# Kernel tuning notes

Hardware: AMD Instinct MI355X
Metric: run time of the kernel (lower is better)

## Reference

```python
import jax, jax.numpy as jnp
import numpy as np

D_MODEL = 1024
NUM_HEADS = 16
HEAD_DIM = D_MODEL // NUM_HEADS  # 64


def setup_inputs() -> dict:
    key = jax.random.key(0)
    ks = jax.random.split(key, 9)
    s = 1.0 / np.sqrt(D_MODEL)
    return {
        "x": jax.random.normal(ks[0], (2, 2048, D_MODEL), dtype=jnp.float32),
        "Wq": jax.random.normal(ks[1], (D_MODEL, D_MODEL), dtype=jnp.float32) * s,
        "bq": jnp.zeros((D_MODEL,), dtype=jnp.float32),
        "Wk": jax.random.normal(ks[2], (D_MODEL, HEAD_DIM), dtype=jnp.float32) * s,
        "bk": jnp.zeros((HEAD_DIM,), dtype=jnp.float32),
        "Wv": jax.random.normal(ks[3], (D_MODEL, HEAD_DIM), dtype=jnp.float32) * s,
        "bv": jnp.zeros((HEAD_DIM,), dtype=jnp.float32),
        "Wo": jax.random.normal(ks[4], (D_MODEL, D_MODEL), dtype=jnp.float32) * s,
        "bo": jnp.zeros((D_MODEL,), dtype=jnp.float32),
    }


def reference(x, Wq, bq, Wk, bk, Wv, bv, Wo, bo):
    B, S, D = x.shape
    H, hd = NUM_HEADS, HEAD_DIM
    # Projections: Q has H heads, K/V a single shared head (MQA).
    Q = (x @ Wq + bq).reshape(B, S, H, hd).transpose(0, 2, 1, 3)  # [B,H,S,hd]
    K = x @ Wk + bk  # [B,S,hd]
    V = x @ Wv + bv  # [B,S,hd]
    # Shared-K/V attention: broadcast K across heads instead of expand().
    scores = jnp.einsum("bhqd,bkd->bhqk", Q, K) / np.sqrt(hd)  # [B,H,S,S]
    attn = jax.nn.softmax(scores, axis=-1)
    attended = jnp.einsum("bhqk,bkd->bhqd", attn, V)  # [B,H,S,hd]
    attended = attended.transpose(0, 2, 1, 3).reshape(B, S, D)
    return attended @ Wo + bo
```

## Files before the change

### kernel.cpp

```cpp
#include <hip/hip_runtime.h>
#include <hip/hip_bf16.h>

#define D_MODEL 1024
#define NHEADS  16
#define HD      64
#define BATCH   2
#define SEQ     2048
#define MROWS   4096
#define NQKV    1152
#define NSPLIT  2

typedef short  short4v __attribute__((ext_vector_type(4)));
typedef short  short8  __attribute__((ext_vector_type(8)));
typedef float  floatx4 __attribute__((ext_vector_type(4)));

__device__ inline short f2bf(float f) {
  unsigned u = __builtin_bit_cast(unsigned, f);
  u = (u + 0x7FFF + ((u >> 16) & 1)) >> 16;
  return (short)u;
}

__device__ inline unsigned pack_trunc(float lo, float hi) {
  return __builtin_amdgcn_perm(__builtin_bit_cast(unsigned, hi),
                               __builtin_bit_cast(unsigned, lo), 0x07060302u);
}

__device__ inline void async_copy16(const short* g, short* l) {
  __builtin_amdgcn_global_load_lds(
      (const __attribute__((address_space(1))) unsigned int*)g,
      (__attribute__((address_space(3))) unsigned int*)l, 16, 0, 0);
}

__global__ __launch_bounds__(256)
void prep_kernel(const float* __restrict__ x,  const float* __restrict__ Wq,
                 const float* __restrict__ Wk, const float* __restrict__ Wv,
                 const float* __restrict__ Wo, const float* __restrict__ bq,
                 const float* __restrict__ bk, const float* __restrict__ bv,
                 short* __restrict__ xb, short* __restrict__ Wqkv_t,
                 short* __restrict__ Wo_t, float* __restrict__ bqkv) {
  const int id = blockIdx.x;
  const int t  = threadIdx.x;
  if (id < 544) {
    __shared__ short Ts[64 * 72];
    const float* src; short* dst; int N, off, tile;
    if (id < 256)      { src = Wq; dst = Wqkv_t; N = 1024; off = 0;    tile = id; }
    else if (id < 272) { src = Wk; dst = Wqkv_t; N = 64;   off = 1024; tile = id - 256; }
    else if (id < 288) { src = Wv; dst = Wqkv_t; N = 64;   off = 1088; tile = id - 272; }
    else               { src = Wo; dst = Wo_t;   N = 1024; off = 0;    tile = id - 288; }
    const int k0 = (N == 1024) ? (tile & 15) * 64 : tile * 64;
    const int n0 = (N == 1024) ? (tile >> 4) * 64 : 0;
    {
      const int r = t >> 2, c = (t & 3) * 16;
      const float* s = src + (size_t)(k0 + r) * N + n0 + c;
#pragma unroll
      for (int j = 0; j < 16; j += 4) {
        float4 v = *reinterpret_cast<const float4*>(s + j);
        Ts[r * 72 + c + j + 0] = f2bf(v.x); Ts[r * 72 + c + j + 1] = f2bf(v.y);
        Ts[r * 72 + c + j + 2] = f2bf(v.z); Ts[r * 72 + c + j + 3] = f2bf(v.w);
      }
    }
    __syncthreads();
    {
      const int n = t >> 2, kc = (t & 3) * 16;
      short8 o0, o1;
#pragma unroll
      for (int j = 0; j < 8; ++j) o0[j] = Ts[(kc + j) * 72 + n];
#pragma unroll
      for (int j = 0; j < 8; ++j) o1[j] = Ts[(kc + 8 + j) * 72 + n];
      short* d = dst + (size_t)(off + n0 + n) * 1024 + k0 + kc;
      *reinterpret_cast<short8*>(d)     = o0;
      *reinterpret_cast<short8*>(d + 8) = o1;
    }
  } else if (id < 549) {
    const int i = (id - 544) * 256 + t;
    if (i < 1024)      bqkv[i] = bq[i];
    else if (i < 1088) bqkv[i] = bk[i - 1024];
    else if (i < 1152) bqkv[i] = bv[i - 1088];
  } else {
    const int i = ((id - 549) * 256 + t) * 8;
    if (i < MROWS * D_MODEL) {
      float4 a = *reinterpret_cast<const float4*>(x + i);
      float4 b = *reinterpret_cast<const float4*>(x + i + 4);
      short8 o;
      o[0] = f2bf(a.x); o[1] = f2bf(a.y); o[2] = f2bf(a.z); o[3] = f2bf(a.w);
      o[4] = f2bf(b.x); o[5] = f2bf(b.y); o[6] = f2bf(b.z); o[7] = f2bf(b.w);
      *reinterpret_cast<short8*>(xb + i) = o;
    }
  }
}

template<bool OUT_BF16, int SCALE_N, bool VT_FUSE>
__global__ __launch_bounds__(256)
void gemm_mfma_bt(const short* __restrict__ A, const short* __restrict__ Bt,
                  const float* __restrict__ bias, void* __restrict__ Cout,
                  short* __restrict__ Vtg, int M, int N, int K) {
  __shared__ short As[128 * 64];
  __shared__ short Bs[64 * 64];
  const int t    = threadIdx.x;
  const int w    = t >> 6;
  const int lane = t & 63;
  const int quad = lane >> 4;
  const int l16  = lane & 15;
  const int bm   = blockIdx.x * 128;
  const int bn   = blockIdx.y * 64;
  const int wm   = (w >> 1) * 64;
  const int wn   = (w & 1) * 32;

  const int srow = t >> 3;
  const int cc   = ((t & 7) ^ (srow & 7)) * 8;
  const short* gA = A  + (size_t)(bm + srow) * K + cc;
  const short* gB = Bt + (size_t)(bn + srow) * K + cc;
  short* lA = As + t * 8;
  short* lB = Bs + t * 8;

  floatx4 acc[4][2];
#pragma unroll
  for (int i = 0; i < 4; ++i)
#pragma unroll
    for (int j = 0; j < 2; ++j) acc[i][j] = (floatx4){0.f, 0.f, 0.f, 0.f};

  const int xr = l16 & 7;

  for (int k0 = 0; k0 < K; k0 += 64) {
    __syncthreads();
    async_copy16(gA + k0, lA);
    async_copy16(gA + (size_t)32 * K + k0, lA + 2048);
    async_copy16(gA + (size_t)64 * K + k0, lA + 4096);
    async_copy16(gA + (size_t)96 * K + k0, lA + 6144);
    async_copy16(gB + k0, lB);
    async_copy16(gB + (size_t)32 * K + k0, lB + 2048);
    __syncthreads();

    short8 fa0[4], fa1[4], fb0[2], fb1[2];
#pragma unroll
    for (int mi = 0; mi < 4; ++mi) {
      const int row = wm + mi * 16 + l16;
      fa0[mi] = *reinterpret_cast<const short8*>(&As[row * 64 + (quad ^ xr) * 8]);
      fa1[mi] = *reinterpret_cast<const short8*>(&As[row * 64 + ((4 + quad) ^ xr) * 8]);
    }
#pragma unroll
    for (int ni = 0; ni < 2; ++ni) {
      const int row = wn + ni * 16 + l16;
      fb0[ni] = *reinterpret_cast<const short8*>(&Bs[row * 64 + (quad ^ xr) * 8]);
      fb1[ni] = *reinterpret_cast<const short8*>(&Bs[row * 64 + ((4 + quad) ^ xr) * 8]);
    }
#pragma unroll
    for (int mi = 0; mi < 4; ++mi)
#pragma unroll
      for (int ni = 0; ni < 2; ++ni) {
        acc[mi][ni] = __builtin_amdgcn_mfma_f32_16x16x32_bf16(fa0[mi], fb0[ni], acc[mi][ni], 0, 0, 0);
        acc[mi][ni] = __builtin_amdgcn_mfma_f32_16x16x32_bf16(fa1[mi], fb1[ni], acc[mi][ni], 0, 0, 0);
      }
  }

#pragma unroll
  for (int ni = 0; ni < 2; ++ni) {
    const int col = bn + wn + ni * 16 + l16;
    const float bs = bias[col];
    const float sc = (col < SCALE_N) ? 0.18033688f : 1.0f;
#pragma unroll
    for (int mi = 0; mi < 4; ++mi) {
      const int row = bm + wm + mi * 16 + quad * 4;
      short4v vt4;
#pragma unroll
      for (int r = 0; r < 4; ++r) {
        const float v = (acc[mi][ni][r] + bs) * sc;
        if (OUT_BF16) {
          const short bv16 = f2bf(v);
          ((short*)Cout)[(size_t)(row + r) * N + col] = bv16;
          if (VT_FUSE) vt4[r] = bv16;
        } else {
          ((float*)Cout)[(size_t)(row + r) * N + col] = v;
        }
      }
      if (VT_FUSE && col >= 1088) {
        const int d = col - 1088;
        const int b = row >> 11, s = row & 2047;
        *reinterpret_cast<short4v*>(&Vtg[(size_t)(b * 64 + d) * SEQ + s]) = vt4;
      }
    }
  }
}

__global__ __launch_bounds__(256, 2)
void mqa_flash_bf16(const short* __restrict__ QKV, const short* __restrict__ Vtg,
                    _Float16* __restrict__ Opart, float* __restrict__ lpart) {
  const int bh    = blockIdx.y;
  const int b     = bh >> 4;
  const int h     = bh & 15;
  const int s0    = blockIdx.x * 256;
  const int split = blockIdx.z;
  const int t     = threadIdx.x;
  const int w     = t >> 6;
  const int lane  = t & 63;
  const int quad  = lane >> 4;
  const int l16   = lane & 15;

  __shared__ short KVs[8192];
  __shared__ short Ps[4 * 16 * 72];
  short* Ks   = KVs;
  short* Vt   = KVs + 4096;
  short* myPs = Ps + w * 16 * 72;

  short8 aq[4][2];
#pragma unroll
  for (int st = 0; st < 4; ++st) {
    const short* qrow = &QKV[(size_t)(b * SEQ + s0 + w * 64 + st * 16 + l16) * NQKV + h * HD];
    aq[st][0] = *reinterpret_cast<const short8*>(qrow + quad * 8);
    aq[st][1] = *reinterpret_cast<const short8*>(qrow + 32 + quad * 8);
  }

  floatx4 oacc[4][4];
  floatx4 lacc[4];
#pragma unroll
  for (int st = 0; st < 4; ++st) {
    lacc[st] = (floatx4){0.f, 0.f, 0.f, 0.f};
#pragma unroll
    for (int dg = 0; dg < 4; ++dg) oacc[st][dg] = (floatx4){0.f, 0.f, 0.f, 0.f};
  }

  short8 ones;
#pragma unroll
  for (int j = 0; j < 8; ++j) ones[j] = (short)0x3F80;

  const int srow = t >> 3;
  const int cc   = ((t & 7) ^ (srow & 7)) * 8;
  const short* gK0 = QKV + (size_t)(b * SEQ + srow) * NQKV + 1024 + cc;
  const short* gK1 = gK0 + (size_t)32 * NQKV;
  const short* gV0 = Vtg + (size_t)(b * 64 + srow) * SEQ + cc;
  const short* gV1 = gV0 + (size_t)32 * SEQ;
  short* lK0 = Ks + w * 512;
  short* lK1 = Ks + 2048 + w * 512;
  short* lV0 = Vt + w * 512;
  short* lV1 = Vt + 2048 + w * 512;

  const int xr = l16 & 7;
  const int kbase = split * (SEQ / NSPLIT);

  for (int kk = kbase; kk < kbase + SEQ / NSPLIT; kk += 64) {
    __syncthreads();
    async_copy16(gK0 + (size_t)kk * NQKV, lK0);
    async_copy16(gK1 + (size_t)kk * NQKV, lK1);
    async_copy16(gV0 + kk, lV0);
    async_copy16(gV1 + kk, lV1);
    __syncthreads();

    short8 kb[4][2], vb[4][2];
#pragma unroll
    for (int kg = 0; kg < 4; ++kg) {
      kb[kg][0] = *reinterpret_cast<const short8*>(&Ks[(kg * 16 + l16) * 64 + (quad ^ xr) * 8]);
      kb[kg][1] = *reinterpret_cast<const short8*>(&Ks[(kg * 16 + l16) * 64 + ((4 + quad) ^ xr) * 8]);
    }
#pragma unroll
    for (int dg = 0; dg < 4; ++dg) {
      vb[dg][0] = *reinterpret_cast<const short8*>(&Vt[(dg * 16 + l16) * 64 + (quad ^ xr) * 8]);
      vb[dg][1] = *reinterpret_cast<const short8*>(&Vt[(dg * 16 + l16) * 64 + ((4 + quad) ^ xr) * 8]);
    }

#pragma unroll
    for (int st = 0; st < 4; ++st) {
#pragma unroll
      for (int kg = 0; kg < 4; ++kg) {
        floatx4 s4 = (floatx4){0.f, 0.f, 0.f, 0.f};
        s4 = __builtin_amdgcn_mfma_f32_16x16x32_bf16(kb[kg][0], aq[st][0], s4, 0, 0, 0);
        s4 = __builtin_amdgcn_mfma_f32_16x16x32_bf16(kb[kg][1], aq[st][1], s4, 0, 0, 0);
        float p0 = __builtin_exp2f(s4[0]);
        float p1 = __builtin_exp2f(s4[1]);
        float p2 = __builtin_exp2f(s4[2]);
        float p3 = __builtin_exp2f(s4[3]);
        uint2 pk;
        pk.x = pack_trunc(p0, p1);
        pk.y = pack_trunc(p2, p3);
        *reinterpret_cast<uint2*>(&myPs[l16 * 72 + kg * 16 + quad * 4]) = pk;
      }
      short8 ap0 = *reinterpret_cast<const short8*>(&myPs[l16 * 72 + quad * 8]);
      short8 ap1 = *reinterpret_cast<const short8*>(&myPs[l16 * 72 + 32 + quad * 8]);
      lacc[st] = __builtin_amdgcn_mfma_f32_16x16x32_bf16(ap0, ones, lacc[st], 0, 0, 0);
      lacc[st] = __builtin_amdgcn_mfma_f32_16x16x32_bf16(ap1, ones, lacc[st], 0, 0, 0);
#pragma unroll
      for (int dg = 0; dg < 4; ++dg) {
        oacc[st][dg] = __builtin_amdgcn_mfma_f32_16x16x32_bf16(ap0, vb[dg][0], oacc[st][dg], 0, 0, 0);
        oacc[st][dg] = __builtin_amdgcn_mfma_f32_16x16x32_bf16(ap1, vb[dg][1], oacc[st][dg], 0, 0, 0);
      }
    }
  }

#pragma unroll
  for (int st = 0; st < 4; ++st) {
#pragma unroll
    for (int rg = 0; rg < 4; ++rg) {
      const int qg = s0 + w * 64 + st * 16 + quad * 4 + rg;
      _Float16* dst = Opart + ((size_t)(split * 32 + bh) * SEQ + qg) * 64 + l16;
#pragma unroll
      for (int dg = 0; dg < 4; ++dg) dst[dg * 16] = (_Float16)oacc[st][dg][rg];
      if (l16 == 0) lpart[(size_t)(split * 32 + bh) * SEQ + qg] = lacc[st][rg];
    }
  }
}

__global__ __launch_bounds__(256)
void combine_kernel(const _Float16* __restrict__ Opart, const float* __restrict__ lpart,
                    short* __restrict__ Att) {
  const int idx = blockIdx.x * 256 + threadIdx.x;
  const int r   = idx >> 3;
  const int d0  = (idx & 7) * 8;
  float l = 0.f;
  float o[8] = {0.f,0.f,0.f,0.f,0.f,0.f,0.f,0.f};
#pragma unroll
  for (int s = 0; s < NSPLIT; ++s) {
    const _Float16* op = Opart + ((size_t)(s * 32 * SEQ) + r) * 64 + d0;
    l += lpart[(size_t)s * 32 * SEQ + r];
#pragma unroll
    for (int j = 0; j < 8; ++j) o[j] += (float)op[j];
  }
  const float inv = 1.0f / l;
  short8 ov;
#pragma unroll
  for (int j = 0; j < 8; ++j) ov[j] = f2bf(o[j] * inv);
  const int bhh = r >> 11, q = r & 2047;
  const int bb = bhh >> 4, hh = bhh & 15;
  *reinterpret_cast<short8*>(&Att[(size_t)(bb * SEQ + q) * D_MODEL + hh * HD + d0]) = ov;
}

extern "C" void kernel_launch(void* const* d_in, const int* in_sizes, int n_in,
                              void* d_out, int out_size, void* d_ws, size_t ws_size,
                              hipStream_t stream) {
  const float* x  = (const float*)d_in[0];
  const float* Wq = (const float*)d_in[1];
  const float* bq = (const float*)d_in[2];
  const float* Wk = (const float*)d_in[3];
  const float* bk = (const float*)d_in[4];
  const float* Wv = (const float*)d_in[5];
  const float* bv = (const float*)d_in[6];
  const float* Wo = (const float*)d_in[7];
  const float* bo = (const float*)d_in[8];
  float* out = (float*)d_out;

  short* Wqkv_t = (short*)d_ws;
  short* Wo_t   = Wqkv_t + (size_t)NQKV * D_MODEL;
  short* xb     = Wo_t + (size_t)D_MODEL * D_MODEL;
  short* QKV    = xb + (size_t)MROWS * D_MODEL;
  short* Att    = QKV + (size_t)MROWS * NQKV;
  short* Vtg    = Att + (size_t)MROWS * D_MODEL;
  float* bqkv   = (float*)(Vtg + (size_t)BATCH * HD * SEQ);
  float* lpart  = bqkv + 1152;
  _Float16* Opart = (_Float16*)(lpart + (size_t)NSPLIT * 32 * SEQ);

  prep_kernel<<<2597, 256, 0, stream>>>(x, Wq, Wk, Wv, Wo, bq, bk, bv,
                                        xb, Wqkv_t, Wo_t, bqkv);

  gemm_mfma_bt<true, 1024, true><<<dim3(MROWS / 128, NQKV / 64), 256, 0, stream>>>(
      xb, Wqkv_t, bqkv, QKV, Vtg, MROWS, NQKV, D_MODEL);

  mqa_flash_bf16<<<dim3(SEQ / 256, BATCH * NHEADS, NSPLIT), 256, 0, stream>>>(
      QKV, Vtg, Opart, lpart);

  combine_kernel<<<2048, 256, 0, stream>>>(Opart, lpart, Att);

  gemm_mfma_bt<false, 0, false><<<dim3(MROWS / 128, D_MODEL / 64), 256, 0, stream>>>(
      Att, Wo_t, bo, out, nullptr, MROWS, D_MODEL, D_MODEL);
}
```

Before: 182.9 us.

## Replace split-K attention and combine kernel with smaller query tiles

Drops the two-way split over the key dimension and its separate combine kernel. Each attention block now covers 128 queries instead of 256 and walks the full key sequence, normalizing and writing bf16 output directly. Launch bounds rise to 4 blocks per CU so the reduced per-thread accumulator state allows more occupancy. This removes the fp16 partial writes, the extra launch and the combine pass, but each K/V tile loaded into LDS is now reused by fewer query rows.

```diff
diff --git a/kernel.cpp b/kernel.cpp
--- a/kernel.cpp
+++ b/kernel.cpp
@@ -8,7 +8,6 @@
 #define SEQ     2048
 #define MROWS   4096
 #define NQKV    1152
-#define NSPLIT  2
 
 typedef short  short4v __attribute__((ext_vector_type(4)));
 typedef short  short8  __attribute__((ext_vector_type(8)));
@@ -182,14 +181,13 @@
   }
 }
 
-__global__ __launch_bounds__(256, 2)
+__global__ __launch_bounds__(256, 4)
 void mqa_flash_bf16(const short* __restrict__ QKV, const short* __restrict__ Vtg,
-                    _Float16* __restrict__ Opart, float* __restrict__ lpart) {
+                    short* __restrict__ Att) {
   const int bh    = blockIdx.y;
   const int b     = bh >> 4;
   const int h     = bh & 15;
-  const int s0    = blockIdx.x * 256;
-  const int split = blockIdx.z;
+  const int s0    = blockIdx.x * 128;
   const int t     = threadIdx.x;
   const int w     = t >> 6;
   const int lane  = t & 63;
@@ -202,18 +200,18 @@
   short* Vt   = KVs + 4096;
   short* myPs = Ps + w * 16 * 72;
 
-  short8 aq[4][2];
-#pragma unroll
-  for (int st = 0; st < 4; ++st) {
-    const short* qrow = &QKV[(size_t)(b * SEQ + s0 + w * 64 + st * 16 + l16) * NQKV + h * HD];
+  short8 aq[2][2];
+#pragma unroll
+  for (int st = 0; st < 2; ++st) {
+    const short* qrow = &QKV[(size_t)(b * SEQ + s0 + w * 32 + st * 16 + l16) * NQKV + h * HD];
     aq[st][0] = *reinterpret_cast<const short8*>(qrow + quad * 8);
     aq[st][1] = *reinterpret_cast<const short8*>(qrow + 32 + quad * 8);
   }
 
-  floatx4 oacc[4][4];
-  floatx4 lacc[4];
-#pragma unroll
-  for (int st = 0; st < 4; ++st) {
+  floatx4 oacc[2][4];
+  floatx4 lacc[2];
+#pragma unroll
+  for (int st = 0; st < 2; ++st) {
     lacc[st] = (floatx4){0.f, 0.f, 0.f, 0.f};
 #pragma unroll
     for (int dg = 0; dg < 4; ++dg) oacc[st][dg] = (floatx4){0.f, 0.f, 0.f, 0.f};
@@ -235,9 +233,8 @@
   short* lV1 = Vt + 2048 + w * 512;
 
   const int xr = l16 & 7;
-  const int kbase = split * (SEQ / NSPLIT);
-
-  for (int kk = kbase; kk < kbase + SEQ / NSPLIT; kk += 64) {
+
+  for (int kk = 0; kk < SEQ; kk += 64) {
     __syncthreads();
     async_copy16(gK0 + (size_t)kk * NQKV, lK0);
     async_copy16(gK1 + (size_t)kk * NQKV, lK1);
@@ -258,7 +255,7 @@
     }
 
 #pragma unroll
-    for (int st = 0; st < 4; ++st) {
+    for (int st = 0; st < 2; ++st) {
 #pragma unroll
       for (int kg = 0; kg < 4; ++kg) {
         floatx4 s4 = (floatx4){0.f, 0.f, 0.f, 0.f};
@@ -286,40 +283,17 @@
   }
 
 #pragma unroll
-  for (int st = 0; st < 4; ++st) {
+  for (int st = 0; st < 2; ++st) {
 #pragma unroll
     for (int rg = 0; rg < 4; ++rg) {
-      const int qg = s0 + w * 64 + st * 16 + quad * 4 + rg;
-      _Float16* dst = Opart + ((size_t)(split * 32 + bh) * SEQ + qg) * 64 + l16;
-#pragma unroll
-      for (int dg = 0; dg < 4; ++dg) dst[dg * 16] = (_Float16)oacc[st][dg][rg];
-      if (l16 == 0) lpart[(size_t)(split * 32 + bh) * SEQ + qg] = lacc[st][rg];
-    }
-  }
-}
-
-__global__ __launch_bounds__(256)
-void combine_kernel(const _Float16* __restrict__ Opart, const float* __restrict__ lpart,
-                    short* __restrict__ Att) {
-  const int idx = blockIdx.x * 256 + threadIdx.x;
-  const int r   = idx >> 3;
-  const int d0  = (idx & 7) * 8;
-  float l = 0.f;
-  float o[8] = {0.f,0.f,0.f,0.f,0.f,0.f,0.f,0.f};
-#pragma unroll
-  for (int s = 0; s < NSPLIT; ++s) {
-    const _Float16* op = Opart + ((size_t)(s * 32 * SEQ) + r) * 64 + d0;
-    l += lpart[(size_t)s * 32 * SEQ + r];
-#pragma unroll
-    for (int j = 0; j < 8; ++j) o[j] += (float)op[j];
-  }
-  const float inv = 1.0f / l;
-  short8 ov;
-#pragma unroll
-  for (int j = 0; j < 8; ++j) ov[j] = f2bf(o[j] * inv);
-  const int bhh = r >> 11, q = r & 2047;
-  const int bb = bhh >> 4, hh = bhh & 15;
-  *reinterpret_cast<short8*>(&Att[(size_t)(bb * SEQ + q) * D_MODEL + hh * HD + d0]) = ov;
+      const float inv = 1.0f / lacc[st][rg];
+      const int qg = s0 + w * 32 + st * 16 + quad * 4 + rg;
+      short* dst = &Att[(size_t)(b * SEQ + qg) * D_MODEL + h * HD + l16];
+#pragma unroll
+      for (int dg = 0; dg < 4; ++dg)
+        dst[dg * 16] = f2bf(oacc[st][dg][rg] * inv);
+    }
+  }
 }
 
 extern "C" void kernel_launch(void* const* d_in, const int* in_sizes, int n_in,
@@ -343,8 +317,6 @@
   short* Att    = QKV + (size_t)MROWS * NQKV;
   short* Vtg    = Att + (size_t)MROWS * D_MODEL;
   float* bqkv   = (float*)(Vtg + (size_t)BATCH * HD * SEQ);
-  float* lpart  = bqkv + 1152;
-  _Float16* Opart = (_Float16*)(lpart + (size_t)NSPLIT * 32 * SEQ);
 
   prep_kernel<<<2597, 256, 0, stream>>>(x, Wq, Wk, Wv, Wo, bq, bk, bv,
                                         xb, Wqkv_t, Wo_t, bqkv);
@@ -352,10 +324,7 @@
   gemm_mfma_bt<true, 1024, true><<<dim3(MROWS / 128, NQKV / 64), 256, 0, stream>>>(
       xb, Wqkv_t, bqkv, QKV, Vtg, MROWS, NQKV, D_MODEL);
 
-  mqa_flash_bf16<<<dim3(SEQ / 256, BATCH * NHEADS, NSPLIT), 256, 0, stream>>>(
-      QKV, Vtg, Opart, lpart);
-
-  combine_kernel<<<2048, 256, 0, stream>>>(Opart, lpart, Att);
+  mqa_flash_bf16<<<dim3(SEQ / 128, BATCH * NHEADS), 256, 0, stream>>>(QKV, Vtg, Att);
 
   gemm_mfma_bt<false, 0, false><<<dim3(MROWS / 128, D_MODEL / 64), 256, 0, stream>>>(
       Att, Wo_t, bo, out, nullptr, MROWS, D_MODEL, D_MODEL);
```

Result: no change. 182.6 us (-0.1%).
